# Optimization experiments

Hardware: AMD Instinct MI355X
Metric: run time of the kernel (lower is better)

Reference implementation:

```python
import jax, jax.numpy as jnp
import numpy as np

# lower-triangular (row, col) positions in the packed order used by the torch loop:
# index order is (j,i) for j in 0..2, i in 0..j -> (0,0),(1,0),(1,1),(2,0),(2,1),(2,2)
_ROWS = jnp.array([0, 1, 1, 2, 2, 2])
_COLS = jnp.array([0, 0, 1, 0, 1, 2])


def setup_inputs() -> dict:
    key = jax.random.key(0)
    bn, seq_len = 4096, 1024
    chol_cov = jax.random.normal(key, (bn, seq_len, 6), dtype=jnp.float32)
    return {"chol_cov": chol_cov}


def reference(chol_cov) -> jnp.ndarray:
    bn, seq_len, _ = chol_cov.shape
    # scatter packed values into lower-triangular 3x3 L: [bn, seq, 3, 3]
    L = jnp.zeros((bn, seq_len, 3, 3), dtype=chol_cov.dtype)
    L = L.at[..., _ROWS, _COLS].set(chol_cov)
    # Q = L @ L^T, batched tiny 3x3 matmul -> symmetric covariance
    Q = jnp.einsum('bsij,bskj->bsik', L, L)
    return Q
```

## Files before the change

kernel.cpp:

```cpp
#include <hip/hip_runtime.h>


#define THREADS 256
#define IPB 1024

typedef float f4 __attribute__((ext_vector_type(4)));

__global__ __launch_bounds__(THREADS) void chol_to_cov_kernel(
    const float* __restrict__ in, float* __restrict__ out, long long n_items) {
  __shared__ float s_in[IPB * 6];

  const int tid = threadIdx.x;
  const long long block_base = (long long)blockIdx.x * IPB;

  if (block_base + IPB <= n_items) {
    const f4* __restrict__ in4 = (const f4*)(in + block_base * 6);
    f4* s4 = (f4*)s_in;
#pragma unroll
    for (int k = 0; k < 6; k++) {
      const int idx = tid + k * THREADS;
      s4[idx] = __builtin_nontemporal_load(&in4[idx]);
    }
    __syncthreads();

    f4* __restrict__ out4 = (f4*)(out + block_base * 9);
#pragma unroll
    for (int k = 0; k < 9; k++) {
      const unsigned g = (unsigned)tid + k * THREADS;
      const unsigned e = 4u * g;
      const unsigned item = e / 9u;
      const unsigned r = e - 9u * item;
      unsigned i1 = item + 1u;
      if (i1 > IPB - 1u) i1 = IPB - 1u;

      const float* p0 = s_in + item * 6;
      const float a = p0[0], b = p0[1], c = p0[2];
      const float d = p0[3], e0 = p0[4], f = p0[5];
      const float u0 = a * a;
      const float u1 = a * b;
      const float u2 = a * d;
      const float u3 = b * b + c * c;
      const float u4 = b * d + c * e0;
      const float u5 = d * d + e0 * e0 + f * f;

      const float* p1 = s_in + i1 * 6;
      const float a1 = p1[0], b1 = p1[1], d1 = p1[3];
      const float v0 = a1 * a1;
      const float v1 = a1 * b1;
      const float v2 = a1 * d1;

      f4 o;
      switch (r) {
        case 0: o = (f4){u0, u1, u2, u1}; break;
        case 1: o = (f4){u1, u2, u1, u3}; break;
        case 2: o = (f4){u2, u1, u3, u4}; break;
        case 3: o = (f4){u1, u3, u4, u2}; break;
        case 4: o = (f4){u3, u4, u2, u4}; break;
        case 5: o = (f4){u4, u2, u4, u5}; break;
        case 6: o = (f4){u2, u4, u5, v0}; break;
        case 7: o = (f4){u4, u5, v0, v1}; break;
        default: o = (f4){u5, v0, v1, v2}; break;
      }
      __builtin_nontemporal_store(o, &out4[g]);
    }
  } else {
    for (long long it = block_base + tid; it < n_items; it += THREADS) {
      const float a = in[it * 6 + 0];
      const float b = in[it * 6 + 1];
      const float c = in[it * 6 + 2];
      const float d = in[it * 6 + 3];
      const float e = in[it * 6 + 4];
      const float f = in[it * 6 + 5];
      float* o = out + it * 9;
      o[0] = a * a;
      o[1] = a * b;
      o[2] = a * d;
      o[3] = a * b;
      o[4] = b * b + c * c;
      o[5] = b * d + c * e;
      o[6] = a * d;
      o[7] = b * d + c * e;
      o[8] = d * d + e * e + f * f;
    }
  }
}

extern "C" void kernel_launch(void* const* d_in, const int* in_sizes, int n_in,
                              void* d_out, int out_size, void* d_ws,
                              size_t ws_size, hipStream_t stream) {
  const float* in = (const float*)d_in[0];
  float* out = (float*)d_out;
  const long long n_items = (long long)in_sizes[0] / 6;
  const long long grid = (n_items + IPB - 1) / IPB;
  chol_to_cov_kernel<<<(int)grid, THREADS, 0, stream>>>(in, out, n_items);
}
```

Measured before the change: 216.4 us.

## Stage output through shared memory and halve items per block

Instead of computing each output float4 directly from packed inputs, with a divide, a switch and redundant recomputation, each thread now computes full 3x3 results for two items into a shared output buffer. The buffer is then streamed out with coalesced float4 nontemporal stores. Items per block drop from 1024 to 512, which keeps shared memory use moderate and doubles the grid. This removes ALU and divergence overhead at the cost of an extra barrier and stride-9 and stride-6 shared memory accesses that may hit bank conflicts.

```diff
diff --git a/kernel.cpp b/kernel.cpp
--- a/kernel.cpp
+++ b/kernel.cpp
@@ -2,66 +2,60 @@
 
 
 #define THREADS 256
-#define IPB 1024
+#define IPB 512
 
 typedef float f4 __attribute__((ext_vector_type(4)));
 
 __global__ __launch_bounds__(THREADS) void chol_to_cov_kernel(
     const float* __restrict__ in, float* __restrict__ out, long long n_items) {
-  __shared__ float s_in[IPB * 6];
+  __shared__ __attribute__((aligned(16))) float s_in[IPB * 6];
+  __shared__ __attribute__((aligned(16))) float s_out[IPB * 9];
 
   const int tid = threadIdx.x;
   const long long block_base = (long long)blockIdx.x * IPB;
 
   if (block_base + IPB <= n_items) {
     const f4* __restrict__ in4 = (const f4*)(in + block_base * 6);
-    f4* s4 = (f4*)s_in;
+    f4* s4i = (f4*)s_in;
 #pragma unroll
-    for (int k = 0; k < 6; k++) {
+    for (int k = 0; k < 3; k++) {
       const int idx = tid + k * THREADS;
-      s4[idx] = __builtin_nontemporal_load(&in4[idx]);
+      s4i[idx] = __builtin_nontemporal_load(&in4[idx]);
+    }
+    __syncthreads();
+
+#pragma unroll
+    for (int t = 0; t < 2; t++) {
+      const int item = tid + t * THREADS;
+      const float* p = s_in + item * 6;
+      const float a = p[0], b = p[1], c = p[2];
+      const float d = p[3], e0 = p[4], f = p[5];
+      const float u1 = a * b;
+      const float u2 = a * d;
+      const float u4 = b * d + c * e0;
+      float* q = s_out + item * 9;
+      q[0] = a * a;
+      q[1] = u1;
+      q[2] = u2;
+      q[3] = u1;
+      q[4] = b * b + c * c;
+      q[5] = u4;
+      q[6] = u2;
+      q[7] = u4;
+      q[8] = d * d + e0 * e0 + f * f;
     }
     __syncthreads();
 
     f4* __restrict__ out4 = (f4*)(out + block_base * 9);
+    const f4* s4o = (const f4*)s_out;
 #pragma unroll
-    for (int k = 0; k < 9; k++) {
-      const unsigned g = (unsigned)tid + k * THREADS;
-      const unsigned e = 4u * g;
-      const unsigned item = e / 9u;
-      const unsigned r = e - 9u * item;
-      unsigned i1 = item + 1u;
-      if (i1 > IPB - 1u) i1 = IPB - 1u;
-
-      const float* p0 = s_in + item * 6;
-      const float a = p0[0], b = p0[1], c = p0[2];
-      const float d = p0[3], e0 = p0[4], f = p0[5];
-      const float u0 = a * a;
-      const float u1 = a * b;
-      const float u2 = a * d;
-      const float u3 = b * b + c * c;
-      const float u4 = b * d + c * e0;
-      const float u5 = d * d + e0 * e0 + f * f;
-
-      const float* p1 = s_in + i1 * 6;
-      const float a1 = p1[0], b1 = p1[1], d1 = p1[3];
-      const float v0 = a1 * a1;
-      const float v1 = a1 * b1;
-      const float v2 = a1 * d1;
-
-      f4 o;
-      switch (r) {
-        case 0: o = (f4){u0, u1, u2, u1}; break;
-        case 1: o = (f4){u1, u2, u1, u3}; break;
-        case 2: o = (f4){u2, u1, u3, u4}; break;
-        case 3: o = (f4){u1, u3, u4, u2}; break;
-        case 4: o = (f4){u3, u4, u2, u4}; break;
-        case 5: o = (f4){u4, u2, u4, u5}; break;
-        case 6: o = (f4){u2, u4, u5, v0}; break;
-        case 7: o = (f4){u4, u5, v0, v1}; break;
-        default: o = (f4){u5, v0, v1, v2}; break;
-      }
-      __builtin_nontemporal_store(o, &out4[g]);
+    for (int k = 0; k < 4; k++) {
+      const int idx = tid + k * THREADS;
+      __builtin_nontemporal_store(s4o[idx], &out4[idx]);
+    }
+    const int idx4 = tid + 4 * THREADS;
+    if (idx4 < (IPB * 9) / 4) {
+      __builtin_nontemporal_store(s4o[idx4], &out4[idx4]);
     }
   } else {
     for (long long it = block_base + tid; it < n_items; it += THREADS) {
```

After: 213.6 us. No clear change (-1.3%).
